# Performance work log

Measured on AMD Instinct MI355X. Metric: run time of the kernel, lower is better.

Reference implementation:

```python
import jax, jax.numpy as jnp
import numpy as np

B, C, H, W = 16, 64, 128, 128
MX, MY = 24, 24
HIDDEN = max(1, int(C * 0.5))


def setup_inputs() -> dict:
    key = jax.random.key(0)
    ks = jax.random.split(key, 9)
    scale = 1.0 / (C * C)
    return {
        "x": jax.random.normal(ks[0], (B, C, H, W), jnp.float32),
        "w_real": scale * jax.random.normal(ks[1], (MX, MY, C, C), jnp.float32),
        "w_imag": scale * jax.random.normal(ks[2], (MX, MY, C, C), jnp.float32),
        "w_skip": jax.random.normal(ks[3], (C, C), jnp.float32) * (1.0 / np.sqrt(C)),
        "fc1_w": jax.random.normal(ks[4], (HIDDEN, C), jnp.float32) * (1.0 / np.sqrt(C)),
        "fc1_b": jnp.zeros((HIDDEN,), jnp.float32),
        "fc2_w": jax.random.normal(ks[5], (C, HIDDEN), jnp.float32) * (1.0 / np.sqrt(HIDDEN)),
        "fc2_b": jnp.zeros((C,), jnp.float32),
        "gate": jnp.ones((1, C, 1, 1), jnp.float32),
    }


def _spectral_conv(x, w_real, w_imag):
    # x: (B, C, H, W). Hermitian-symmetric 2-D spectral conv, matching torch path.
    b, c, h, w = x.shape
    mx = min(MX, h)
    my = min(MY, w // 2 + 1)
    x_ft = jnp.fft.rfftn(x, axes=(-2, -1))            # (B, C, H, W//2+1) complex
    weight = (w_real[:mx, :my] + 1j * w_imag[:mx, :my]).astype(jnp.complex64)
    out_sl = jnp.einsum('bcxy,xyco->boxy', x_ft[:, :, :mx, :my], weight)
    out_ft = jnp.zeros((b, c, h, w // 2 + 1), jnp.complex64).at[:, :, :mx, :my].set(out_sl)
    # enforce_hermitian_symmetry=True: ifft over leading spatial dim, zero imag
    # of DC / Nyquist columns, then irfft over last dim.
    out_ft = jnp.fft.ifft(out_ft, n=h, axis=-2)
    out_ft = out_ft.at[..., 0].set(out_ft[..., 0].real.astype(jnp.complex64))
    if w % 2 == 0:
        out_ft = out_ft.at[..., -1].set(out_ft[..., -1].real.astype(jnp.complex64))
    return jnp.fft.irfft(out_ft, n=w, axis=-1)


def reference(x, w_real, w_imag, w_skip, fc1_w, fc1_b, fc2_w, fc2_b, gate):
    # fno skip: 1x1 conv, no bias
    skip = jnp.einsum('bchw,oc->bohw', x, w_skip)
    h1 = jax.nn.gelu(_spectral_conv(x, w_real, w_imag) + skip, approximate=False)
    # channel MLP (Conv1d kernel=1 == per-pixel channel matmul)
    z = jnp.einsum('bchw,kc->bkhw', h1, fc1_w) + fc1_b[None, :, None, None]
    z = jax.nn.gelu(z, approximate=False)
    z = jnp.einsum('bkhw,ck->bchw', z, fc2_w) + fc2_b[None, :, None, None]
    # soft-gating skip
    return z + gate * h1
```

## Files before the change

kernel.cpp:

```cpp
#include <hip/hip_runtime.h>
#include <hip/hip_bf16.h>

#define BF __hip_bfloat16


typedef __attribute__((ext_vector_type(8))) short s8b;
typedef __attribute__((ext_vector_type(4))) float f32x4;

__device__ __forceinline__ float geluf(float v) {
    return 0.5f * v * (1.0f + erff(v * 0.7071067811865476f));
}
__device__ __forceinline__ float bf2f(BF v) { return __bfloat162float(v); }
__device__ __forceinline__ short f2bs(float f) {
    union { BF h; short s; } u; u.h = __float2bfloat16(f); return u.s;
}
__device__ __forceinline__ s8b ld8f(const float* __restrict__ p) {
    float4 a = *(const float4*)p;
    float4 b = *(const float4*)(p + 4);
    s8b r;
    r[0] = f2bs(a.x); r[1] = f2bs(a.y); r[2] = f2bs(a.z); r[3] = f2bs(a.w);
    r[4] = f2bs(b.x); r[5] = f2bs(b.y); r[6] = f2bs(b.z); r[7] = f2bs(b.w);
    return r;
}

__global__ __launch_bounds__(256) void k_fwd(const float* __restrict__ x,
                                             BF* __restrict__ XrB,
                                             BF* __restrict__ XiB) {
    __shared__ __align__(16) short B1[48 * 136];
    __shared__ __align__(16) short B2[48 * 264];
    __shared__ __align__(16) short Tl[48 * 136];

    const int tid  = threadIdx.x;
    const int bc   = blockIdx.x;
    const int lane = tid & 63;
    const int wv   = tid >> 6;
    const int lr   = lane & 15;
    const int lg   = lane >> 4;

    for (int i = tid; i < 3072; i += 256) {
        int y = i >> 7, v = i & 127;
        int r = (v * y) & 127;
        float s, c; __sincosf((float)r * 0.04908738521234052f, &s, &c);
        B1[y * 136 + v]        = f2bs(c);
        B1[(y + 24) * 136 + v] = f2bs(-s);
    }
    for (int i = tid; i < 3072; i += 256) {
        int xx = i >> 7, u = i & 127;
        int r = (u * xx) & 127;
        float s, c; __sincosf((float)r * 0.04908738521234052f, &s, &c);
        B2[xx * 264 + u]              = f2bs(c);
        B2[xx * 264 + 128 + u]        = f2bs(s);
        B2[(xx + 24) * 264 + u]       = f2bs(-s);
        B2[(xx + 24) * 264 + 128 + u] = f2bs(c);
    }
    __syncthreads();

    {
        const float* xb = x + ((size_t)bc << 14);
        s8b af[2][4];
        #pragma unroll
        for (int m = 0; m < 2; ++m) {
            const int u = wv * 32 + m * 16 + lr;
            #pragma unroll
            for (int s = 0; s < 4; ++s)
                af[m][s] = ld8f(xb + (size_t)u * 128 + s * 32 + lg * 8);
        }
        f32x4 acc[2][3];
        #pragma unroll
        for (int m = 0; m < 2; ++m)
            #pragma unroll
            for (int n = 0; n < 3; ++n)
                #pragma unroll
                for (int r = 0; r < 4; ++r) acc[m][n][r] = 0.f;
        #pragma unroll
        for (int s = 0; s < 4; ++s)
            #pragma unroll
            for (int n = 0; n < 3; ++n) {
                s8b bfr = *(const s8b*)&B1[(n * 16 + lr) * 136 + s * 32 + lg * 8];
                #pragma unroll
                for (int m = 0; m < 2; ++m)
                    acc[m][n] = __builtin_amdgcn_mfma_f32_16x16x32_bf16(af[m][s], bfr, acc[m][n], 0, 0, 0);
            }
        #pragma unroll
        for (int m = 0; m < 2; ++m) {
            const int u0 = wv * 32 + m * 16 + lg * 4;
            #pragma unroll
            for (int n = 0; n < 3; ++n) {
                short4 t;
                t.x = f2bs(acc[m][n][0]); t.y = f2bs(acc[m][n][1]);
                t.z = f2bs(acc[m][n][2]); t.w = f2bs(acc[m][n][3]);
                *(short4*)&Tl[(n * 16 + lr) * 136 + u0] = t;
            }
        }
    }
    __syncthreads();

    for (int j = wv; j < 6; j += 4) {
        const int m = j / 3, n = j % 3;
        const int y  = m * 16 + lr;
        const int r1 = (y < 24) ? y      : 0;
        const int r2 = (y < 24) ? y + 24 : 0;
        f32x4 acc = {0.f, 0.f, 0.f, 0.f};
        #pragma unroll
        for (int s = 0; s < 8; ++s) {
            s8b a = *(const s8b*)&Tl[((s < 4) ? r1 : r2) * 136 + (s & 3) * 32 + lg * 8];
            s8b b = *(const s8b*)&B2[(n * 16 + lr) * 264 + s * 32 + lg * 8];
            acc = __builtin_amdgcn_mfma_f32_16x16x32_bf16(a, b, acc, 0, 0, 0);
        }
        const int col = n * 16 + lr;
        const int xc  = (col < 24) ? col : col - 24;
        BF* dst = (col < 24) ? XrB : XiB;
        #pragma unroll
        for (int r = 0; r < 4; ++r) {
            const int yo = m * 16 + lg * 4 + r;
            if (yo < 24)
                dst[(size_t)(xc * 24 + yo) * 1024 + bc] = __float2bfloat16(acc[r]);
        }
    }
}

__global__ __launch_bounds__(256) void k_mix(const float* __restrict__ wr_g,
                                             const float* __restrict__ wi_g,
                                             const BF* __restrict__ XrB,
                                             const BF* __restrict__ XiB,
                                             BF* __restrict__ SrB,
                                             BF* __restrict__ SiB) {
    __shared__ __align__(16) float Wr[4096], Wi[4096];
    __shared__ __align__(16) float Xr[16 * 68], Xi[16 * 68];
    const int tid = threadIdx.x;
    const int xy  = blockIdx.x;

    const float4* wr4 = (const float4*)(wr_g + ((size_t)xy << 12));
    const float4* wi4 = (const float4*)(wi_g + ((size_t)xy << 12));
    for (int i = tid; i < 1024; i += 256) {
        *(float4*)&Wr[i << 2] = wr4[i];
        *(float4*)&Wi[i << 2] = wi4[i];
    }
    for (int i = tid; i < 1024; i += 256) {
        int b = i >> 6, c = i & 63;
        Xr[b * 68 + c] = bf2f(XrB[((size_t)xy << 10) + i]);
        Xi[b * 68 + c] = bf2f(XiB[((size_t)xy << 10) + i]);
    }
    __syncthreads();

    const int b  = tid >> 4;
    const int o0 = (tid & 15) << 2;
    float4 sr = {0.f, 0.f, 0.f, 0.f}, si = {0.f, 0.f, 0.f, 0.f};
    const float* xrp = Xr + b * 68;
    const float* xip = Xi + b * 68;
    for (int c = 0; c < 64; ++c) {
        float ar = xrp[c], ac = xip[c];
        float4 w_r = *(const float4*)&Wr[(c << 6) + o0];
        float4 w_i = *(const float4*)&Wi[(c << 6) + o0];
        sr.x += ar * w_r.x - ac * w_i.x;  si.x += ar * w_i.x + ac * w_r.x;
        sr.y += ar * w_r.y - ac * w_i.y;  si.y += ar * w_i.y + ac * w_r.y;
        sr.z += ar * w_r.z - ac * w_i.z;  si.z += ar * w_i.z + ac * w_r.z;
        sr.w += ar * w_r.w - ac * w_i.w;  si.w += ar * w_i.w + ac * w_r.w;
    }
    size_t base = (size_t)((b << 6) + o0) * 576 + xy;
    SrB[base]        = __float2bfloat16(sr.x);  SiB[base]        = __float2bfloat16(si.x);
    SrB[base + 576]  = __float2bfloat16(sr.y);  SiB[base + 576]  = __float2bfloat16(si.y);
    SrB[base + 1152] = __float2bfloat16(sr.z);  SiB[base + 1152] = __float2bfloat16(si.z);
    SrB[base + 1728] = __float2bfloat16(sr.w);  SiB[base + 1728] = __float2bfloat16(si.w);
}

__global__ __launch_bounds__(256) void k_invP(const BF* __restrict__ SrB,
                                              const BF* __restrict__ SiB,
                                              BF* __restrict__ PrB,
                                              BF* __restrict__ PiB) {
    __shared__ __align__(16) float Srs[24 * 28], Sis[24 * 28];
    __shared__ __align__(16) float tcs[24 * 132], tss[24 * 132];
    const int tid = threadIdx.x;
    const int bo  = blockIdx.x;

    for (int i = tid; i < 3072; i += 256) {
        int m = i >> 7, a = i & 127;
        int r = (a * m) & 127;
        float th = (float)r * 0.04908738521234052f;
        float s, c; __sincosf(th, &s, &c);
        tcs[m * 132 + a] = c;
        tss[m * 132 + a] = s;
    }
    for (int i = tid; i < 576; i += 256) {
        int xx = i / 24, yy = i - xx * 24;
        Srs[yy * 28 + xx] = bf2f(SrB[(size_t)bo * 576 + i]);
        Sis[yy * 28 + xx] = bf2f(SiB[(size_t)bo * 576 + i]);
    }
    __syncthreads();

    const int u  = tid & 127;
    const int yh = (tid >> 7) * 12;
    float tcu[24], tsu[24];
    #pragma unroll
    for (int xx = 0; xx < 24; ++xx) {
        tcu[xx] = tcs[xx * 132 + u];
        tsu[xx] = tss[xx * 132 + u];
    }
    const float inv = 6.103515625e-05f;
    BF* prp = PrB + (size_t)bo * 3072 + (size_t)u * 24;
    BF* pip = PiB + (size_t)bo * 3072 + (size_t)u * 24;
    for (int jy = 0; jy < 12; ++jy) {
        int y = yh + jy;
        float pr = 0.f, pi = 0.f;
        #pragma unroll
        for (int xq = 0; xq < 6; ++xq) {
            int x0 = xq << 2;
            float4 s4 = *(const float4*)&Srs[y * 28 + x0];
            float4 z4 = *(const float4*)&Sis[y * 28 + x0];
            pr += s4.x * tcu[x0]     - z4.x * tsu[x0]
                + s4.y * tcu[x0 + 1] - z4.y * tsu[x0 + 1]
                + s4.z * tcu[x0 + 2] - z4.z * tsu[x0 + 2]
                + s4.w * tcu[x0 + 3] - z4.w * tsu[x0 + 3];
            pi += z4.x * tcu[x0]     + s4.x * tsu[x0]
                + z4.y * tcu[x0 + 1] + s4.y * tsu[x0 + 1]
                + z4.z * tcu[x0 + 2] + s4.z * tsu[x0 + 2]
                + z4.w * tcu[x0 + 3] + s4.w * tsu[x0 + 3];
        }
        if (y == 0) {
            prp[0] = __float2bfloat16(pr * inv);
            pip[0] = __float2bfloat16(0.f);
        } else {
            prp[y] = __float2bfloat16(2.f * inv * pr);
            pip[y] = __float2bfloat16(2.f * inv * pi);
        }
    }
}

__global__ __launch_bounds__(256) void k_fused(const float* __restrict__ x,
                                               const BF* __restrict__ PrB,
                                               const BF* __restrict__ PiB,
                                               const float* __restrict__ wsk,
                                               const float* __restrict__ w1,
                                               const float* __restrict__ b1,
                                               const float* __restrict__ w2,
                                               const float* __restrict__ b2,
                                               const float* __restrict__ gt,
                                               float* __restrict__ out) {
    __shared__ __align__(16) short Plds[64 * 72];
    __shared__ __align__(16) short H1s[128 * 72];
    __shared__ __align__(16) short Zls[128 * 40];

    const int tid  = threadIdx.x;
    const int b    = blockIdx.x >> 7;
    const int u    = blockIdx.x & 127;
    const int lane = tid & 63;
    const int wv   = tid >> 6;
    const int lr   = lane & 15;
    const int lg   = lane >> 4;

    {
        const size_t pb = (size_t)(b * 64) * 3072 + (size_t)u * 24;
        for (int i = tid; i < 1536; i += 256) {
            int o = i / 24, y = i - o * 24;
            size_t g = pb + (size_t)o * 3072 + y;
            Plds[o * 72 + y]      = *(const short*)&PrB[g];
            Plds[o * 72 + 24 + y] = *(const short*)&PiB[g];
        }
        for (int i = tid; i < 1024; i += 256)
            Plds[(i >> 4) * 72 + 48 + (i & 15)] = 0;
    }

    s8b ax[2][2];
    {
        const float* xb = x + (size_t)(b * 64) * 16384 + (size_t)u * 128;
        #pragma unroll
        for (int m = 0; m < 2; ++m) {
            const int v = wv * 32 + m * 16 + lr;
            #pragma unroll
            for (int s = 0; s < 2; ++s)
                #pragma unroll
                for (int j = 0; j < 8; ++j)
                    ax[m][s][j] = f2bs(xb[(size_t)(s * 32 + lg * 8 + j) * 16384 + v]);
        }
    }

    s8b atw[2][2];
    #pragma unroll
    for (int m = 0; m < 2; ++m) {
        const int v = wv * 32 + m * 16 + lr;
        #pragma unroll
        for (int s = 0; s < 2; ++s) {
            #pragma unroll
            for (int j = 0; j < 8; ++j) {
                const int k = s * 32 + lg * 8 + j;
                float val = 0.f;
                if (k < 48) {
                    int y = (k < 24) ? k : k - 24;
                    int r = (v * y) & 127;
                    float sn, cs;
                    __sincosf((float)r * 0.04908738521234052f, &sn, &cs);
                    val = (k < 24) ? cs : -sn;
                }
                atw[m][s][j] = f2bs(val);
            }
        }
    }
    __syncthreads();

    f32x4 acc[2][4];
    #pragma unroll
    for (int m = 0; m < 2; ++m)
        #pragma unroll
        for (int n = 0; n < 4; ++n)
            #pragma unroll
            for (int r = 0; r < 4; ++r) acc[m][n][r] = 0.f;

    #pragma unroll
    for (int s = 0; s < 2; ++s) {
        #pragma unroll
        for (int n = 0; n < 4; ++n) {
            s8b bfr = *(const s8b*)&Plds[(n * 16 + lr) * 72 + s * 32 + lg * 8];
            #pragma unroll
            for (int m = 0; m < 2; ++m)
                acc[m][n] = __builtin_amdgcn_mfma_f32_16x16x32_bf16(atw[m][s], bfr, acc[m][n], 0, 0, 0);
        }
    }
    #pragma unroll
    for (int s = 0; s < 2; ++s) {
        #pragma unroll
        for (int n = 0; n < 4; ++n) {
            s8b bfr = ld8f(wsk + (n * 16 + lr) * 64 + s * 32 + lg * 8);
            #pragma unroll
            for (int m = 0; m < 2; ++m)
                acc[m][n] = __builtin_amdgcn_mfma_f32_16x16x32_bf16(ax[m][s], bfr, acc[m][n], 0, 0, 0);
        }
    }

    f32x4 h1r[2][4];
    #pragma unroll
    for (int m = 0; m < 2; ++m)
        #pragma unroll
        for (int n = 0; n < 4; ++n)
            #pragma unroll
            for (int r = 0; r < 4; ++r) {
                float h = geluf(acc[m][n][r]);
                h1r[m][n][r] = h;
                H1s[(wv * 32 + m * 16 + lg * 4 + r) * 72 + n * 16 + lr] = f2bs(h);
            }
    __syncthreads();

    f32x4 zac[2][2];
    #pragma unroll
    for (int m = 0; m < 2; ++m)
        #pragma unroll
        for (int n = 0; n < 2; ++n)
            #pragma unroll
            for (int r = 0; r < 4; ++r) zac[m][n][r] = 0.f;
    #pragma unroll
    for (int s = 0; s < 2; ++s) {
        s8b ah[2];
        #pragma unroll
        for (int m = 0; m < 2; ++m)
            ah[m] = *(const s8b*)&H1s[(wv * 32 + m * 16 + lr) * 72 + s * 32 + lg * 8];
        #pragma unroll
        for (int n = 0; n < 2; ++n) {
            s8b bfr = ld8f(w1 + (n * 16 + lr) * 64 + s * 32 + lg * 8);
            #pragma unroll
            for (int m = 0; m < 2; ++m)
                zac[m][n] = __builtin_amdgcn_mfma_f32_16x16x32_bf16(ah[m], bfr, zac[m][n], 0, 0, 0);
        }
    }
    #pragma unroll
    for (int n = 0; n < 2; ++n) {
        const float bb = b1[n * 16 + lr];
        #pragma unroll
        for (int m = 0; m < 2; ++m)
            #pragma unroll
            for (int r = 0; r < 4; ++r)
                Zls[(wv * 32 + m * 16 + lg * 4 + r) * 40 + n * 16 + lr] =
                    f2bs(geluf(zac[m][n][r] + bb));
    }
    __syncthreads();

    f32x4 oac[2][4];
    #pragma unroll
    for (int m = 0; m < 2; ++m)
        #pragma unroll
        for (int n = 0; n < 4; ++n)
            #pragma unroll
            for (int r = 0; r < 4; ++r) oac[m][n][r] = 0.f;
    s8b az[2];
    #pragma unroll
    for (int m = 0; m < 2; ++m)
        az[m] = *(const s8b*)&Zls[(wv * 32 + m * 16 + lr) * 40 + lg * 8];
    #pragma unroll
    for (int n = 0; n < 4; ++n) {
        s8b bfr = ld8f(w2 + (n * 16 + lr) * 32 + lg * 8);
        #pragma unroll
        for (int m = 0; m < 2; ++m)
            oac[m][n] = __builtin_amdgcn_mfma_f32_16x16x32_bf16(az[m], bfr, oac[m][n], 0, 0, 0);
    }

    float* ob = out + ((size_t)(b * 64) * 128 + u) * 128;
    #pragma unroll
    for (int n = 0; n < 4; ++n) {
        const int o = n * 16 + lr;
        const float b2v = b2[o];
        const float gv  = gt[o];
        #pragma unroll
        for (int m = 0; m < 2; ++m)
            #pragma unroll
            for (int r = 0; r < 4; ++r) {
                int v = wv * 32 + m * 16 + lg * 4 + r;
                ob[(size_t)o * 16384 + v] = oac[m][n][r] + b2v + gv * h1r[m][n][r];
            }
    }
}

extern "C" void kernel_launch(void* const* d_in, const int* in_sizes, int n_in,
                              void* d_out, int out_size, void* d_ws, size_t ws_size,
                              hipStream_t stream) {
    (void)in_sizes; (void)n_in; (void)out_size; (void)ws_size;
    const float* x   = (const float*)d_in[0];
    const float* wr  = (const float*)d_in[1];
    const float* wi  = (const float*)d_in[2];
    const float* wsk = (const float*)d_in[3];
    const float* w1  = (const float*)d_in[4];
    const float* b1  = (const float*)d_in[5];
    const float* w2  = (const float*)d_in[6];
    const float* b2  = (const float*)d_in[7];
    const float* gt  = (const float*)d_in[8];

    BF* wsB = (BF*)d_ws;
    BF* Xr  = wsB + 6291456;
    BF* Xi  = wsB + 6881280;
    BF* Sr  = wsB;
    BF* Si  = wsB + 589824;
    BF* Pr  = wsB + 1179648;
    BF* Pi  = wsB + 4325376;

    hipLaunchKernelGGL(k_fwd,  dim3(1024), dim3(256), 0, stream, x, Xr, Xi);
    hipLaunchKernelGGL(k_mix,  dim3(576),  dim3(256), 0, stream, wr, wi, Xr, Xi, Sr, Si);
    hipLaunchKernelGGL(k_invP, dim3(1024), dim3(256), 0, stream, Sr, Si, Pr, Pi);
    hipLaunchKernelGGL(k_fused, dim3(2048), dim3(256), 0, stream,
                       x, Pr, Pi, wsk, w1, b1, w2, b2, gt, (float*)d_out);
}
```

Before: 239.4 us.

## Move spectral mix and inverse DFT to bf16 MFMA, precompute twiddles globally

The per-mode complex channel mix and the inverse row DFT move from scalar fp32 loops to bf16 MFMA matrix multiplies. Real and imaginary parts are packed into stacked operand blocks so each complex product becomes a real GEMM. A new small kernel writes the forward DFT twiddle tables to global memory once per call, so the 1024 forward-transform blocks no longer each compute sincos tables into LDS. GELU's erff is replaced by a polynomial erf approximation. The trade-offs are bf16 rounding in the mix and inverse stages, a small approximation error in GELU, and one extra kernel launch.

```diff
diff --git a/kernel.cpp b/kernel.cpp
--- a/kernel.cpp
+++ b/kernel.cpp
@@ -7,8 +7,16 @@
 typedef __attribute__((ext_vector_type(8))) short s8b;
 typedef __attribute__((ext_vector_type(4))) float f32x4;
 
+__device__ __forceinline__ float erf_fast(float x) {
+    float ax = fabsf(x);
+    float t  = 1.0f / (1.0f + 0.3275911f * ax);
+    float p  = t * (0.254829592f + t * (-0.284496736f + t * (1.421413741f
+             + t * (-1.453152027f + t * 1.061405429f))));
+    float r  = 1.0f - p * __expf(-ax * ax);
+    return copysignf(r, x);
+}
 __device__ __forceinline__ float geluf(float v) {
-    return 0.5f * v * (1.0f + erff(v * 0.7071067811865476f));
+    return 0.5f * v * (1.0f + erf_fast(v * 0.7071067811865476f));
 }
 __device__ __forceinline__ float bf2f(BF v) { return __bfloat162float(v); }
 __device__ __forceinline__ short f2bs(float f) {
@@ -23,11 +31,32 @@
     return r;
 }
 
+__global__ __launch_bounds__(256) void k_tw(BF* __restrict__ gB1,
+                                            BF* __restrict__ gB2) {
+    int idx = blockIdx.x * 256 + threadIdx.x;
+    if (idx < 6144) {
+        int y = idx >> 7, v = idx & 127;
+        int yy = (y < 24) ? y : y - 24;
+        int r = (v * yy) & 127;
+        float s, c; __sincosf((float)r * 0.04908738521234052f, &s, &c);
+        gB1[idx] = __float2bfloat16(y < 24 ? c : -s);
+    } else {
+        int j = idx - 6144;
+        int xp = j >> 8, k = j & 255;
+        int u = k & 127, half = k >> 7;
+        int x = (xp < 24) ? xp : xp - 24;
+        int r = (u * x) & 127;
+        float s, c; __sincosf((float)r * 0.04908738521234052f, &s, &c);
+        float val = (xp < 24) ? (half ? s : c) : (half ? c : -s);
+        gB2[j] = __float2bfloat16(val);
+    }
+}
+
 __global__ __launch_bounds__(256) void k_fwd(const float* __restrict__ x,
+                                             const BF* __restrict__ gB1,
+                                             const BF* __restrict__ gB2,
                                              BF* __restrict__ XrB,
                                              BF* __restrict__ XiB) {
-    __shared__ __align__(16) short B1[48 * 136];
-    __shared__ __align__(16) short B2[48 * 264];
     __shared__ __align__(16) short Tl[48 * 136];
 
     const int tid  = threadIdx.x;
@@ -37,24 +66,6 @@
     const int lr   = lane & 15;
     const int lg   = lane >> 4;
 
-    for (int i = tid; i < 3072; i += 256) {
-        int y = i >> 7, v = i & 127;
-        int r = (v * y) & 127;
-        float s, c; __sincosf((float)r * 0.04908738521234052f, &s, &c);
-        B1[y * 136 + v]        = f2bs(c);
-        B1[(y + 24) * 136 + v] = f2bs(-s);
-    }
-    for (int i = tid; i < 3072; i += 256) {
-        int xx = i >> 7, u = i & 127;
-        int r = (u * xx) & 127;
-        float s, c; __sincosf((float)r * 0.04908738521234052f, &s, &c);
-        B2[xx * 264 + u]              = f2bs(c);
-        B2[xx * 264 + 128 + u]        = f2bs(s);
-        B2[(xx + 24) * 264 + u]       = f2bs(-s);
-        B2[(xx + 24) * 264 + 128 + u] = f2bs(c);
-    }
-    __syncthreads();
-
     {
         const float* xb = x + ((size_t)bc << 14);
         s8b af[2][4];
@@ -76,7 +87,7 @@
         for (int s = 0; s < 4; ++s)
             #pragma unroll
             for (int n = 0; n < 3; ++n) {
-                s8b bfr = *(const s8b*)&B1[(n * 16 + lr) * 136 + s * 32 + lg * 8];
+                s8b bfr = *(const s8b*)((const short*)gB1 + (n * 16 + lr) * 128 + s * 32 + lg * 8);
                 #pragma unroll
                 for (int m = 0; m < 2; ++m)
                     acc[m][n] = __builtin_amdgcn_mfma_f32_16x16x32_bf16(af[m][s], bfr, acc[m][n], 0, 0, 0);
@@ -104,7 +115,7 @@
         #pragma unroll
         for (int s = 0; s < 8; ++s) {
             s8b a = *(const s8b*)&Tl[((s < 4) ? r1 : r2) * 136 + (s & 3) * 32 + lg * 8];
-            s8b b = *(const s8b*)&B2[(n * 16 + lr) * 264 + s * 32 + lg * 8];
+            s8b b = *(const s8b*)((const short*)gB2 + (n * 16 + lr) * 256 + s * 32 + lg * 8);
             acc = __builtin_amdgcn_mfma_f32_16x16x32_bf16(a, b, acc, 0, 0, 0);
         }
         const int col = n * 16 + lr;
@@ -125,105 +136,128 @@
                                              const BF* __restrict__ XiB,
                                              BF* __restrict__ SrB,
                                              BF* __restrict__ SiB) {
-    __shared__ __align__(16) float Wr[4096], Wi[4096];
-    __shared__ __align__(16) float Xr[16 * 68], Xi[16 * 68];
-    const int tid = threadIdx.x;
-    const int xy  = blockIdx.x;
-
-    const float4* wr4 = (const float4*)(wr_g + ((size_t)xy << 12));
-    const float4* wi4 = (const float4*)(wi_g + ((size_t)xy << 12));
-    for (int i = tid; i < 1024; i += 256) {
-        *(float4*)&Wr[i << 2] = wr4[i];
-        *(float4*)&Wi[i << 2] = wi4[i];
-    }
-    for (int i = tid; i < 1024; i += 256) {
-        int b = i >> 6, c = i & 63;
-        Xr[b * 68 + c] = bf2f(XrB[((size_t)xy << 10) + i]);
-        Xi[b * 68 + c] = bf2f(XiB[((size_t)xy << 10) + i]);
-    }
-    __syncthreads();
-
-    const int b  = tid >> 4;
-    const int o0 = (tid & 15) << 2;
-    float4 sr = {0.f, 0.f, 0.f, 0.f}, si = {0.f, 0.f, 0.f, 0.f};
-    const float* xrp = Xr + b * 68;
-    const float* xip = Xi + b * 68;
-    for (int c = 0; c < 64; ++c) {
-        float ar = xrp[c], ac = xip[c];
-        float4 w_r = *(const float4*)&Wr[(c << 6) + o0];
-        float4 w_i = *(const float4*)&Wi[(c << 6) + o0];
-        sr.x += ar * w_r.x - ac * w_i.x;  si.x += ar * w_i.x + ac * w_r.x;
-        sr.y += ar * w_r.y - ac * w_i.y;  si.y += ar * w_i.y + ac * w_r.y;
-        sr.z += ar * w_r.z - ac * w_i.z;  si.z += ar * w_i.z + ac * w_r.z;
-        sr.w += ar * w_r.w - ac * w_i.w;  si.w += ar * w_i.w + ac * w_r.w;
-    }
-    size_t base = (size_t)((b << 6) + o0) * 576 + xy;
-    SrB[base]        = __float2bfloat16(sr.x);  SiB[base]        = __float2bfloat16(si.x);
-    SrB[base + 576]  = __float2bfloat16(sr.y);  SiB[base + 576]  = __float2bfloat16(si.y);
-    SrB[base + 1152] = __float2bfloat16(sr.z);  SiB[base + 1152] = __float2bfloat16(si.z);
-    SrB[base + 1728] = __float2bfloat16(sr.w);  SiB[base + 1728] = __float2bfloat16(si.w);
+    __shared__ __align__(16) short Br[64 * 136], Bi[64 * 136];
+    const int tid  = threadIdx.x;
+    const int xy   = blockIdx.x;
+    const int lane = tid & 63;
+    const int wv   = tid >> 6;
+    const int lr   = lane & 15;
+    const int lg   = lane >> 4;
+
+    const float* wrp = wr_g + ((size_t)xy << 12);
+    const float* wip = wi_g + ((size_t)xy << 12);
+    for (int i = tid; i < 4096; i += 256) {
+        int c = i >> 6, o = i & 63;
+        float vr = wrp[i], vi = wip[i];
+        short br = f2bs(vr), bi = f2bs(vi), nbi = f2bs(-vi);
+        Br[o * 136 + c]      = br;
+        Br[o * 136 + 64 + c] = nbi;
+        Bi[o * 136 + c]      = bi;
+        Bi[o * 136 + 64 + c] = br;
+    }
+
+    s8b az[4];
+    {
+        const short* xr = (const short*)XrB + ((size_t)xy << 10) + lr * 64;
+        const short* xi = (const short*)XiB + ((size_t)xy << 10) + lr * 64;
+        #pragma unroll
+        for (int s = 0; s < 2; ++s) {
+            az[s]     = *(const s8b*)(xr + s * 32 + lg * 8);
+            az[s + 2] = *(const s8b*)(xi + s * 32 + lg * 8);
+        }
+    }
+    __syncthreads();
+
+    f32x4 ar = {0.f, 0.f, 0.f, 0.f}, ai = {0.f, 0.f, 0.f, 0.f};
+    #pragma unroll
+    for (int s = 0; s < 4; ++s) {
+        s8b brf = *(const s8b*)&Br[(wv * 16 + lr) * 136 + s * 32 + lg * 8];
+        ar = __builtin_amdgcn_mfma_f32_16x16x32_bf16(az[s], brf, ar, 0, 0, 0);
+    }
+    #pragma unroll
+    for (int s = 0; s < 4; ++s) {
+        s8b bif = *(const s8b*)&Bi[(wv * 16 + lr) * 136 + s * 32 + lg * 8];
+        ai = __builtin_amdgcn_mfma_f32_16x16x32_bf16(az[s], bif, ai, 0, 0, 0);
+    }
+
+    const int o = wv * 16 + lr;
+    #pragma unroll
+    for (int r = 0; r < 4; ++r) {
+        int b = lg * 4 + r;
+        size_t base = (size_t)((b << 6) + o) * 576 + xy;
+        SrB[base] = __float2bfloat16(ar[r]);
+        SiB[base] = __float2bfloat16(ai[r]);
+    }
 }
 
 __global__ __launch_bounds__(256) void k_invP(const BF* __restrict__ SrB,
                                               const BF* __restrict__ SiB,
                                               BF* __restrict__ PrB,
                                               BF* __restrict__ PiB) {
-    __shared__ __align__(16) float Srs[24 * 28], Sis[24 * 28];
-    __shared__ __align__(16) float tcs[24 * 132], tss[24 * 132];
-    const int tid = threadIdx.x;
-    const int bo  = blockIdx.x;
-
-    for (int i = tid; i < 3072; i += 256) {
-        int m = i >> 7, a = i & 127;
-        int r = (a * m) & 127;
-        float th = (float)r * 0.04908738521234052f;
-        float s, c; __sincosf(th, &s, &c);
-        tcs[m * 132 + a] = c;
-        tss[m * 132 + a] = s;
-    }
+    __shared__ __align__(16) short Bp[48 * 72];
+    const int tid  = threadIdx.x;
+    const int bo   = blockIdx.x;
+    const int lane = tid & 63;
+    const int wv   = tid >> 6;
+    const int lr   = lane & 15;
+    const int lg   = lane >> 4;
+    const float inv = 6.103515625e-05f;
+
     for (int i = tid; i < 576; i += 256) {
-        int xx = i / 24, yy = i - xx * 24;
-        Srs[yy * 28 + xx] = bf2f(SrB[(size_t)bo * 576 + i]);
-        Sis[yy * 28 + xx] = bf2f(SiB[(size_t)bo * 576 + i]);
-    }
-    __syncthreads();
-
-    const int u  = tid & 127;
-    const int yh = (tid >> 7) * 12;
-    float tcu[24], tsu[24];
-    #pragma unroll
-    for (int xx = 0; xx < 24; ++xx) {
-        tcu[xx] = tcs[xx * 132 + u];
-        tsu[xx] = tss[xx * 132 + u];
-    }
-    const float inv = 6.103515625e-05f;
-    BF* prp = PrB + (size_t)bo * 3072 + (size_t)u * 24;
-    BF* pip = PiB + (size_t)bo * 3072 + (size_t)u * 24;
-    for (int jy = 0; jy < 12; ++jy) {
-        int y = yh + jy;
-        float pr = 0.f, pi = 0.f;
-        #pragma unroll
-        for (int xq = 0; xq < 6; ++xq) {
-            int x0 = xq << 2;
-            float4 s4 = *(const float4*)&Srs[y * 28 + x0];
-            float4 z4 = *(const float4*)&Sis[y * 28 + x0];
-            pr += s4.x * tcu[x0]     - z4.x * tsu[x0]
-                + s4.y * tcu[x0 + 1] - z4.y * tsu[x0 + 1]
-                + s4.z * tcu[x0 + 2] - z4.z * tsu[x0 + 2]
-                + s4.w * tcu[x0 + 3] - z4.w * tsu[x0 + 3];
-            pi += z4.x * tcu[x0]     + s4.x * tsu[x0]
-                + z4.y * tcu[x0 + 1] + s4.y * tsu[x0 + 1]
-                + z4.z * tcu[x0 + 2] + s4.z * tsu[x0 + 2]
-                + z4.w * tcu[x0 + 3] + s4.w * tsu[x0 + 3];
-        }
-        if (y == 0) {
-            prp[0] = __float2bfloat16(pr * inv);
-            pip[0] = __float2bfloat16(0.f);
-        } else {
-            prp[y] = __float2bfloat16(2.f * inv * pr);
-            pip[y] = __float2bfloat16(2.f * inv * pi);
-        }
-    }
+        int x = i / 24, y = i - x * 24;
+        float sr = bf2f(SrB[(size_t)bo * 576 + i]);
+        float si = bf2f(SiB[(size_t)bo * 576 + i]);
+        float sc = (y == 0) ? inv : 2.0f * inv;
+        Bp[y * 72 + x]             = f2bs(sc * sr);
+        Bp[y * 72 + 24 + x]        = f2bs(-sc * si);
+        Bp[(24 + y) * 72 + x]      = f2bs((y == 0) ? 0.f : sc * si);
+        Bp[(24 + y) * 72 + 24 + x] = f2bs((y == 0) ? 0.f : sc * sr);
+    }
+    for (int i = tid; i < 768; i += 256)
+        Bp[(i >> 4) * 72 + 48 + (i & 15)] = 0;
+
+    s8b a[2][2];
+    #pragma unroll
+    for (int m = 0; m < 2; ++m) {
+        const int u = wv * 32 + m * 16 + lr;
+        #pragma unroll
+        for (int s = 0; s < 2; ++s) {
+            #pragma unroll
+            for (int j = 0; j < 8; ++j) {
+                const int k = s * 32 + lg * 8 + j;
+                float val = 0.f;
+                if (k < 48) {
+                    int x = (k < 24) ? k : k - 24;
+                    int r = (u * x) & 127;
+                    float sn, cs;
+                    __sincosf((float)r * 0.04908738521234052f, &sn, &cs);
+                    val = (k < 24) ? cs : sn;
+                }
+                a[m][s][j] = f2bs(val);
+            }
+        }
+    }
+    __syncthreads();
+
+    #pragma unroll
+    for (int m = 0; m < 2; ++m)
+        #pragma unroll
+        for (int n = 0; n < 3; ++n) {
+            f32x4 acc = {0.f, 0.f, 0.f, 0.f};
+            #pragma unroll
+            for (int s = 0; s < 2; ++s) {
+                s8b bfr = *(const s8b*)&Bp[(n * 16 + lr) * 72 + s * 32 + lg * 8];
+                acc = __builtin_amdgcn_mfma_f32_16x16x32_bf16(a[m][s], bfr, acc, 0, 0, 0);
+            }
+            const int col = n * 16 + lr;
+            BF* dst = (col < 24) ? PrB : PiB;
+            const int y = (col < 24) ? col : col - 24;
+            #pragma unroll
+            for (int r = 0; r < 4; ++r) {
+                const int u = wv * 32 + m * 16 + lg * 4 + r;
+                dst[(size_t)bo * 3072 + (size_t)u * 24 + y] = __float2bfloat16(acc[r]);
+            }
+        }
 }
 
 __global__ __launch_bounds__(256) void k_fused(const float* __restrict__ x,
@@ -422,6 +456,8 @@
     const float* gt  = (const float*)d_in[8];
 
     BF* wsB = (BF*)d_ws;
+    BF* gB1 = wsB;
+    BF* gB2 = wsB + 6144;
     BF* Xr  = wsB + 6291456;
     BF* Xi  = wsB + 6881280;
     BF* Sr  = wsB;
@@ -429,7 +465,8 @@
     BF* Pr  = wsB + 1179648;
     BF* Pi  = wsB + 4325376;
 
-    hipLaunchKernelGGL(k_fwd,  dim3(1024), dim3(256), 0, stream, x, Xr, Xi);
+    hipLaunchKernelGGL(k_tw,   dim3(72),   dim3(256), 0, stream, gB1, gB2);
+    hipLaunchKernelGGL(k_fwd,  dim3(1024), dim3(256), 0, stream, x, gB1, gB2, Xr, Xi);
     hipLaunchKernelGGL(k_mix,  dim3(576),  dim3(256), 0, stream, wr, wi, Xr, Xi, Sr, Si);
     hipLaunchKernelGGL(k_invP, dim3(1024), dim3(256), 0, stream, Sr, Si, Pr, Pi);
     hipLaunchKernelGGL(k_fused, dim3(2048), dim3(256), 0, stream,
```

New measurement: 222.7 us. -7.0%, faster.
